# Optimization experiments

Measured on AMD Instinct MI355X. Metric: run time of the kernel, lower is better.

Reference implementation:

```python
import jax, jax.numpy as jnp
import numpy as np

EMBED_DIM = 1024
NUM_HEADS = 16
HEAD_DIM = EMBED_DIM // NUM_HEADS


def setup_inputs() -> dict:
    key = jax.random.key(0)
    ks = jax.random.split(key, 7)
    B, S, E = 2, 2048, EMBED_DIM
    # xavier_uniform bound for square [E, E] weight
    bound = float(np.sqrt(6.0 / (E + E)))
    mkw = lambda k: jax.random.uniform(k, (E, E), jnp.float32, -bound, bound)
    return {
        "query": jax.random.normal(ks[0], (B, S, E), jnp.float32),
        "key": jax.random.normal(ks[1], (B, S, E), jnp.float32),
        "value": jax.random.normal(ks[2], (B, S, E), jnp.float32),
        "Wq": mkw(ks[3]),
        "Wk": mkw(ks[4]),
        "Wv": mkw(ks[5]),
        "Wo": mkw(ks[6]),
    }


def reference(query, key, value, Wq, Wk, Wv, Wo):
    # Chunked sigmoid attention: since sigmoid has no cross-key normalization
    # and all projections are bias-free linear maps, summing per-KV-chunk
    # partial outputs is mathematically identical to the full computation:
    #   out = (sigmoid(scale * Q K^T) @ V) @ Wo^T
    B, L, E = query.shape
    H, D = NUM_HEADS, HEAD_DIM
    scale = D ** -0.5
    q = (query @ Wq.T).reshape(B, L, H, D) * scale   # [B,L,H,D]
    k = (key @ Wk.T).reshape(B, -1, H, D)            # [B,S,H,D]
    v = (value @ Wv.T).reshape(B, -1, H, D)          # [B,S,H,D]
    scores = jax.nn.sigmoid(jnp.einsum('blhd,bshd->bhls', q, k))  # [B,H,L,S]
    o = jnp.einsum('bhls,bshd->blhd', scores, v).reshape(B, L, E)
    return o @ Wo.T
```

## Files before the change

kernel.cpp:

```cpp
#include <hip/hip_runtime.h>

typedef float f32x4 __attribute__((ext_vector_type(4)));
typedef float f32x16 __attribute__((ext_vector_type(16)));
typedef __bf16 bf16x4 __attribute__((ext_vector_type(4)));
typedef __bf16 bf16x8 __attribute__((ext_vector_type(8)));

constexpr int E = 1024;
constexpr int S = 2048;
constexpr int Bsz = 2;
constexpr int H = 16;
constexpr int Dh = 64;
constexpr int M = Bsz * S;

#define GLOAD_LDS16(g, l)                                                                 \
  __builtin_amdgcn_global_load_lds((const __attribute__((address_space(1))) void*)(g),    \
                                   (__attribute__((address_space(3))) void*)(l), 16, 0, 0)

__device__ __forceinline__ unsigned pk2(float a, float b) {
  union { __bf16 h[2]; unsigned u; } r;
  r.h[0] = (__bf16)a; r.h[1] = (__bf16)b;
  return r.u;
}

__global__ __launch_bounds__(256) void convert_bf16(
    const float* __restrict__ q, const float* __restrict__ k,
    const float* __restrict__ v, const float* __restrict__ wq,
    const float* __restrict__ wk, const float* __restrict__ wv,
    const float* __restrict__ wo, __bf16* __restrict__ aq,
    __bf16* __restrict__ ak, __bf16* __restrict__ av,
    __bf16* __restrict__ wqkv, __bf16* __restrict__ wob) {
  const int id = blockIdx.y;
  const float* src;
  __bf16* dst;
  int n;
  float scale = 1.0f;
  switch (id) {
    case 0: src = q;  dst = aq;             n = M * E; break;
    case 1: src = k;  dst = ak;             n = M * E; break;
    case 2: src = v;  dst = av;             n = M * E; break;
    case 3: src = wq; dst = wqkv;           n = E * E; scale = -0.18033688f; break;
    case 4: src = wk; dst = wqkv + E * E;   n = E * E; break;
    case 5: src = wv; dst = wqkv + 2 * E * E; n = E * E; break;
    default: src = wo; dst = wob;           n = E * E; break;
  }
  const int stride = gridDim.x * 256 * 8;
  for (int i = (blockIdx.x * 256 + threadIdx.x) * 8; i < n; i += stride) {
    f32x4 a = *reinterpret_cast<const f32x4*>(&src[i]);
    f32x4 b = *reinterpret_cast<const f32x4*>(&src[i + 4]);
    bf16x8 o;
    o[0] = (__bf16)(a[0] * scale); o[1] = (__bf16)(a[1] * scale);
    o[2] = (__bf16)(a[2] * scale); o[3] = (__bf16)(a[3] * scale);
    o[4] = (__bf16)(b[0] * scale); o[5] = (__bf16)(b[1] * scale);
    o[6] = (__bf16)(b[2] * scale); o[7] = (__bf16)(b[3] * scale);
    *reinterpret_cast<bf16x8*>(&dst[i]) = o;
  }
}

template <int TM, int MODE>
__global__ __launch_bounds__(256) void gemm_bf16nt(
    const __bf16* __restrict__ A0, const __bf16* __restrict__ A1,
    const __bf16* __restrict__ A2, const __bf16* __restrict__ Bw,
    void* __restrict__ C0, void* __restrict__ C1, void* __restrict__ C2) {
  constexpr int MI = TM / 32;
  __shared__ __bf16 As[TM][64];
  __shared__ __bf16 Bs[128][64];

  const int t    = threadIdx.x;
  const int lane = t & 63;
  const int wid  = t >> 6;
  const int wr   = (wid >> 1) * (TM / 2);
  const int wc   = (wid & 1) * 64;
  const int r16  = lane & 15;
  const int tm   = blockIdx.y * TM;
  const int tn   = blockIdx.x * 128;
  const int which = tn >> 10;

  const __bf16* Ab = (MODE == 0) ? (which == 0 ? A0 : which == 1 ? A1 : A2) : A0;

  f32x4 acc[MI][4] = {};

  for (int kt = 0; kt < E / 64; ++kt) {
    const int k0 = kt * 64;
    __syncthreads();
    constexpr int ACH = TM / 8;
    constexpr int NCH = ACH + 16;
#pragma unroll
    for (int c = wid; c < NCH; c += 4) {
      const bool isA = c < ACH;
      const int cc   = isA ? c : c - ACH;
      const int L    = cc * 1024 + lane * 16;
      const int row  = L >> 7;
      const int sw   = ((L >> 4) & 7) ^ (row & 7);
      const __bf16* src = isA ? &Ab[(size_t)(tm + row) * E + k0 + sw * 8]
                              : &Bw[(size_t)(tn + row) * E + k0 + sw * 8];
      char* dst = (isA ? (char*)As : (char*)Bs) + cc * 1024;
      GLOAD_LDS16(src, dst);
    }
    __syncthreads();
#pragma unroll
    for (int kc = 0; kc < 2; ++kc) {
      bf16x8 af[MI], bfv[4];
#pragma unroll
      for (int mi = 0; mi < MI; ++mi) {
        int row = wr + mi * 16 + r16;
        int g   = (kc * 4 + (lane >> 4)) ^ (row & 7);
        af[mi] = *reinterpret_cast<const bf16x8*>(&As[row][g * 8]);
      }
#pragma unroll
      for (int ni = 0; ni < 4; ++ni) {
        int row = wc + ni * 16 + r16;
        int g   = (kc * 4 + (lane >> 4)) ^ (row & 7);
        bfv[ni] = *reinterpret_cast<const bf16x8*>(&Bs[row][g * 8]);
      }
#pragma unroll
      for (int mi = 0; mi < MI; ++mi)
#pragma unroll
        for (int ni = 0; ni < 4; ++ni)
          acc[mi][ni] = __builtin_amdgcn_mfma_f32_16x16x32_bf16(af[mi], bfv[ni],
                                                                acc[mi][ni], 0, 0, 0);
    }
  }

#pragma unroll
  for (int mi = 0; mi < MI; ++mi) {
#pragma unroll
    for (int ni = 0; ni < 4; ++ni) {
#pragma unroll
      for (int j = 0; j < 4; ++j) {
        float v = acc[mi][ni][j];
        int m = tm + wr + mi * 16 + ((lane >> 4) << 2) + j;
        int n = tn + wc + ni * 16 + r16;
        if constexpr (MODE == 0) {
          int nl = n & 1023;
          int b = m >> 11, s = m & 2047, h = nl >> 6, d = nl & 63;
          __bf16* Cout = which == 0 ? (__bf16*)C0 : which == 1 ? (__bf16*)C1
                                                              : (__bf16*)C2;
          if (which < 2) {
            Cout[((size_t)(b * H + h) * S + s) * Dh + d] = (__bf16)v;
          } else {
            int ssw = (s & ~12) | ((s & 4) << 1) | ((s & 8) >> 1);
            Cout[((size_t)(b * H + h) * Dh + d) * S + ssw] = (__bf16)v;
          }
        } else {
          ((float*)C0)[(size_t)m * E + n] = v;
        }
      }
    }
  }
}

__global__ __launch_bounds__(128) void attn_sigmoid(const __bf16* __restrict__ Q,
                                                    const __bf16* __restrict__ K,
                                                    const __bf16* __restrict__ Vt,
                                                    __bf16* __restrict__ O) {
  __shared__ char smem[2][16384];

  const int t    = threadIdx.x;
  const int lane = t & 63;
  const int wid  = t >> 6;
  const int l31  = lane & 31;
  const int hh   = lane >> 5;
  const int q0   = blockIdx.x * 64;
  const int h    = blockIdx.y;
  const int b    = blockIdx.z;

  const __bf16* Qh = Q + (size_t)(b * H + h) * S * Dh;
  const __bf16* Kh = K + (size_t)(b * H + h) * S * Dh;
  const __bf16* Vh = Vt + (size_t)(b * H + h) * Dh * S;

  auto stage = [&](int st, int pb) {
    char* bK = &smem[pb][0];
    char* bV = &smem[pb][8192];
#pragma unroll
    for (int j = 0; j < 4; ++j) {
      int base = (wid * 4 + j) * 1024;
      int L    = base + lane * 16;
      int row  = L >> 7;
      int sw   = ((L >> 4) & 7) ^ (row & 7);
      GLOAD_LDS16(&Kh[(size_t)(st * 64 + row) * Dh + sw * 8], bK + base);
      GLOAD_LDS16(&Vh[(size_t)row * S + st * 64 + sw * 8], bV + base);
    }
  };

  stage(0, 0);

  bf16x8 Qf[4];
#pragma unroll
  for (int kc = 0; kc < 4; ++kc)
    Qf[kc] = *reinterpret_cast<const bf16x8*>(
        &Qh[(size_t)(q0 + wid * 32 + l31) * Dh + kc * 16 + hh * 8]);

  f32x16 ot0 = {}, ot1 = {};
  __syncthreads();

  for (int st = 0; st < S / 64; ++st) {
    const int cur = st & 1;
    if (st + 1 < S / 64) stage(st + 1, cur ^ 1);

    const __bf16* Ks = (const __bf16*)&smem[cur][0];
    const __bf16* Vs = (const __bf16*)(&smem[cur][8192]);

    f32x16 s0 = {}, s1 = {};
    __builtin_amdgcn_s_setprio(1);
#pragma unroll
    for (int kc = 0; kc < 4; ++kc) {
      int x = (2 * kc + hh) ^ (l31 & 7);
      bf16x8 k0 = *reinterpret_cast<const bf16x8*>(&Ks[l31 * 64 + x * 8]);
      bf16x8 k1 = *reinterpret_cast<const bf16x8*>(&Ks[(32 + l31) * 64 + x * 8]);
      s0 = __builtin_amdgcn_mfma_f32_32x32x16_bf16(k0, Qf[kc], s0, 0, 0, 0);
      s1 = __builtin_amdgcn_mfma_f32_32x32x16_bf16(k1, Qf[kc], s1, 0, 0, 0);
    }
    __builtin_amdgcn_s_setprio(0);

    bf16x8 vf[8];
#pragma unroll
    for (int c = 0; c < 4; ++c) {
#pragma unroll
      for (int dblk = 0; dblk < 2; ++dblk) {
        int row = dblk * 32 + l31;
        int x   = (2 * c + hh) ^ (row & 7);
        vf[c * 2 + dblk] = *reinterpret_cast<const bf16x8*>(&Vs[row * 64 + x * 8]);
      }
    }

    bf16x8 F[4];
    {
      union { unsigned u[4]; bf16x8 v; } fu[4];
#pragma unroll
      for (int c = 0; c < 4; ++c) {
        int base = (c & 1) * 8;
#pragma unroll
        for (int jj = 0; jj < 4; ++jj) {
          float ya = (c < 2) ? s0[base + 2 * jj] : s1[base + 2 * jj];
          float yb = (c < 2) ? s0[base + 2 * jj + 1] : s1[base + 2 * jj + 1];
          float pa = __builtin_amdgcn_rcpf(1.0f + __builtin_amdgcn_exp2f(ya));
          float pb = __builtin_amdgcn_rcpf(1.0f + __builtin_amdgcn_exp2f(yb));
          fu[c].u[jj] = pk2(pa, pb);
        }
        F[c] = fu[c].v;
      }
    }

    __builtin_amdgcn_s_setprio(1);
#pragma unroll
    for (int c = 0; c < 4; ++c) {
      ot0 = __builtin_amdgcn_mfma_f32_32x32x16_bf16(vf[c * 2 + 0], F[c], ot0, 0, 0, 0);
      ot1 = __builtin_amdgcn_mfma_f32_32x32x16_bf16(vf[c * 2 + 1], F[c], ot1, 0, 0, 0);
    }
    __builtin_amdgcn_s_setprio(0);

    __syncthreads();
  }

  __bf16* Os = (__bf16*)&smem[0][0];
  {
    int row = wid * 32 + l31;
#pragma unroll
    for (int dblk = 0; dblk < 2; ++dblk) {
#pragma unroll
      for (int rp = 0; rp < 4; ++rp) {
        int r  = rp * 4;
        int g  = dblk * 4 + rp;
        int by = row * 128 + ((g ^ (row & 7)) * 16) + hh * 8;
        float a0 = dblk ? ot1[r]     : ot0[r];
        float a1 = dblk ? ot1[r + 1] : ot0[r + 1];
        float a2 = dblk ? ot1[r + 2] : ot0[r + 2];
        float a3 = dblk ? ot1[r + 3] : ot0[r + 3];
        unsigned long long val =
            (unsigned long long)pk2(a0, a1) | ((unsigned long long)pk2(a2, a3) << 32);
        *reinterpret_cast<unsigned long long*>((char*)Os + by) = val;
      }
    }
  }
  __syncthreads();
#pragma unroll
  for (int i = 0; i < 4; ++i) {
    int c   = i * 128 + t;
    int row = c >> 3;
    int ch  = c & 7;
    bf16x8 v = *reinterpret_cast<const bf16x8*>(
        (char*)Os + row * 128 + ((ch ^ (row & 7)) * 16));
    *reinterpret_cast<bf16x8*>(&O[((size_t)(b * S) + q0 + row) * E + h * Dh + ch * 8]) = v;
  }
}

extern "C" void kernel_launch(void* const* d_in, const int* in_sizes, int n_in,
                              void* d_out, int out_size, void* d_ws, size_t ws_size,
                              hipStream_t stream) {
  const float* query = (const float*)d_in[0];
  const float* key_  = (const float*)d_in[1];
  const float* value = (const float*)d_in[2];
  const float* Wq    = (const float*)d_in[3];
  const float* Wk    = (const float*)d_in[4];
  const float* Wv    = (const float*)d_in[5];
  const float* Wo    = (const float*)d_in[6];

  char* ws = (char*)d_ws;
  __bf16* aq   = (__bf16*)(ws);
  __bf16* ak   = (__bf16*)(ws + ((size_t)8 << 20));
  __bf16* av   = (__bf16*)(ws + ((size_t)16 << 20));
  __bf16* wqkv = (__bf16*)(ws + ((size_t)24 << 20));
  __bf16* wob  = (__bf16*)(ws + ((size_t)30 << 20));
  __bf16* pq   = (__bf16*)(ws + ((size_t)32 << 20));
  __bf16* pk   = (__bf16*)(ws + ((size_t)40 << 20));
  __bf16* pvt  = (__bf16*)(ws + ((size_t)48 << 20));
  __bf16* ob   = (__bf16*)(ws);

  convert_bf16<<<dim3(512, 7), 256, 0, stream>>>(query, key_, value, Wq, Wk, Wv,
                                                 Wo, aq, ak, av, wqkv, wob);

  gemm_bf16nt<128, 0><<<dim3(3072 / 128, M / 128), 256, 0, stream>>>(
      aq, ak, av, wqkv, pq, pk, pvt);

  attn_sigmoid<<<dim3(S / 64, H, Bsz), 128, 0, stream>>>(pq, pk, pvt, ob);

  gemm_bf16nt<64, 2><<<dim3(E / 128, M / 64), 256, 0, stream>>>(
      ob, nullptr, nullptr, wob, (float*)d_out, nullptr, nullptr);
}
```

Before: 154.3 us.

## Split attention key range across two wave pairs and reduce partial outputs in LDS

The attention block grows from 2 to 4 waves. Each pair of waves handles half of the key sequence in 32-key steps, and within a pair one wave loads K while the other loads V. At the end the partial outputs are summed through shared memory. This is meant to raise the number of resident waves and hide latency within each block, at the cost of a cross-wave reduction and smaller MFMA batches per iteration.

```diff
diff --git a/kernel.cpp b/kernel.cpp
--- a/kernel.cpp
+++ b/kernel.cpp
@@ -149,36 +149,44 @@
   }
 }
 
-__global__ __launch_bounds__(128) void attn_sigmoid(const __bf16* __restrict__ Q,
+__global__ __launch_bounds__(256) void attn_sigmoid(const __bf16* __restrict__ Q,
                                                     const __bf16* __restrict__ K,
                                                     const __bf16* __restrict__ Vt,
                                                     __bf16* __restrict__ O) {
-  __shared__ char smem[2][16384];
-
-  const int t    = threadIdx.x;
-  const int lane = t & 63;
-  const int wid  = t >> 6;
-  const int l31  = lane & 31;
-  const int hh   = lane >> 5;
-  const int q0   = blockIdx.x * 64;
-  const int h    = blockIdx.y;
-  const int b    = blockIdx.z;
+  __shared__ char smem[32768];
+
+  const int t     = threadIdx.x;
+  const int lane  = t & 63;
+  const int wid   = t >> 6;
+  const int l31   = lane & 31;
+  const int hh    = lane >> 5;
+  const int qgrp  = wid & 1;
+  const int shalf = wid >> 1;
+  const int q0    = blockIdx.x * 64;
+  const int h     = blockIdx.y;
+  const int b     = blockIdx.z;
 
   const __bf16* Qh = Q + (size_t)(b * H + h) * S * Dh;
   const __bf16* Kh = K + (size_t)(b * H + h) * S * Dh;
   const __bf16* Vh = Vt + (size_t)(b * H + h) * Dh * S;
 
-  auto stage = [&](int st, int pb) {
-    char* bK = &smem[pb][0];
-    char* bV = &smem[pb][8192];
-#pragma unroll
-    for (int j = 0; j < 4; ++j) {
-      int base = (wid * 4 + j) * 1024;
-      int L    = base + lane * 16;
-      int row  = L >> 7;
-      int sw   = ((L >> 4) & 7) ^ (row & 7);
-      GLOAD_LDS16(&Kh[(size_t)(st * 64 + row) * Dh + sw * 8], bK + base);
-      GLOAD_LDS16(&Vh[(size_t)row * S + st * 64 + sw * 8], bV + base);
+  char* const myBase = smem + shalf * 16384;
+
+  const __bf16* kSrc = Kh + (size_t)(shalf * 1024 + (lane >> 3)) * Dh +
+                       (((lane & 7) ^ (lane >> 3)) * 8);
+  const __bf16* vSrc = Vh + (size_t)(lane >> 2) * S + shalf * 1024 +
+                       (((lane & 3) ^ ((lane >> 3) & 3)) * 8);
+
+  auto stage = [&](int it, int buf) {
+    char* dst = myBase + buf * 8192;
+    if (qgrp == 0) {
+#pragma unroll
+      for (int j = 0; j < 4; ++j)
+        GLOAD_LDS16(kSrc + it * 2048 + j * 512, dst + j * 1024);
+    } else {
+#pragma unroll
+      for (int j = 0; j < 4; ++j)
+        GLOAD_LDS16(vSrc + it * 32 + (size_t)j * 16 * S, dst + 4096 + j * 1024);
     }
   };
 
@@ -188,75 +196,110 @@
 #pragma unroll
   for (int kc = 0; kc < 4; ++kc)
     Qf[kc] = *reinterpret_cast<const bf16x8*>(
-        &Qh[(size_t)(q0 + wid * 32 + l31) * Dh + kc * 16 + hh * 8]);
+        &Qh[(size_t)(q0 + qgrp * 32 + l31) * Dh + kc * 16 + hh * 8]);
 
   f32x16 ot0 = {}, ot1 = {};
   __syncthreads();
 
-  for (int st = 0; st < S / 64; ++st) {
-    const int cur = st & 1;
-    if (st + 1 < S / 64) stage(st + 1, cur ^ 1);
-
-    const __bf16* Ks = (const __bf16*)&smem[cur][0];
-    const __bf16* Vs = (const __bf16*)(&smem[cur][8192]);
-
-    f32x16 s0 = {}, s1 = {};
-    __builtin_amdgcn_s_setprio(1);
+#pragma unroll 2
+  for (int it = 0; it < 32; ++it) {
+    const int buf = it & 1;
+    if (it + 1 < 32) stage(it + 1, buf ^ 1);
+
+    const __bf16* Kb = (const __bf16*)(myBase + buf * 8192);
+    const __bf16* Vb = (const __bf16*)(myBase + buf * 8192 + 4096);
+
+    bf16x8 kf[4], vf[4];
 #pragma unroll
     for (int kc = 0; kc < 4; ++kc) {
       int x = (2 * kc + hh) ^ (l31 & 7);
-      bf16x8 k0 = *reinterpret_cast<const bf16x8*>(&Ks[l31 * 64 + x * 8]);
-      bf16x8 k1 = *reinterpret_cast<const bf16x8*>(&Ks[(32 + l31) * 64 + x * 8]);
-      s0 = __builtin_amdgcn_mfma_f32_32x32x16_bf16(k0, Qf[kc], s0, 0, 0, 0);
-      s1 = __builtin_amdgcn_mfma_f32_32x32x16_bf16(k1, Qf[kc], s1, 0, 0, 0);
-    }
-    __builtin_amdgcn_s_setprio(0);
-
-    bf16x8 vf[8];
-#pragma unroll
-    for (int c = 0; c < 4; ++c) {
+      kf[kc] = *reinterpret_cast<const bf16x8*>(&Kb[l31 * 64 + x * 8]);
+    }
+#pragma unroll
+    for (int kc2 = 0; kc2 < 2; ++kc2)
 #pragma unroll
       for (int dblk = 0; dblk < 2; ++dblk) {
         int row = dblk * 32 + l31;
-        int x   = (2 * c + hh) ^ (row & 7);
-        vf[c * 2 + dblk] = *reinterpret_cast<const bf16x8*>(&Vs[row * 64 + x * 8]);
-      }
-    }
-
-    bf16x8 F[4];
+        int x   = (2 * kc2 + hh) ^ ((l31 >> 1) & 3);
+        vf[kc2 * 2 + dblk] = *reinterpret_cast<const bf16x8*>(&Vb[row * 32 + x * 8]);
+      }
+
+    f32x16 sacc = {};
+    __builtin_amdgcn_s_setprio(1);
+#pragma unroll
+    for (int kc = 0; kc < 4; ++kc)
+      sacc = __builtin_amdgcn_mfma_f32_32x32x16_bf16(kf[kc], Qf[kc], sacc, 0, 0, 0);
+    __builtin_amdgcn_s_setprio(0);
+
+    bf16x8 F[2];
     {
-      union { unsigned u[4]; bf16x8 v; } fu[4];
-#pragma unroll
-      for (int c = 0; c < 4; ++c) {
-        int base = (c & 1) * 8;
+      union { unsigned u[4]; bf16x8 v; } fu[2];
+#pragma unroll
+      for (int kc2 = 0; kc2 < 2; ++kc2) {
 #pragma unroll
         for (int jj = 0; jj < 4; ++jj) {
-          float ya = (c < 2) ? s0[base + 2 * jj] : s1[base + 2 * jj];
-          float yb = (c < 2) ? s0[base + 2 * jj + 1] : s1[base + 2 * jj + 1];
+          float ya = sacc[kc2 * 8 + 2 * jj];
+          float yb = sacc[kc2 * 8 + 2 * jj + 1];
           float pa = __builtin_amdgcn_rcpf(1.0f + __builtin_amdgcn_exp2f(ya));
           float pb = __builtin_amdgcn_rcpf(1.0f + __builtin_amdgcn_exp2f(yb));
-          fu[c].u[jj] = pk2(pa, pb);
+          fu[kc2].u[jj] = pk2(pa, pb);
         }
-        F[c] = fu[c].v;
+        F[kc2] = fu[kc2].v;
       }
     }
 
     __builtin_amdgcn_s_setprio(1);
-#pragma unroll
-    for (int c = 0; c < 4; ++c) {
-      ot0 = __builtin_amdgcn_mfma_f32_32x32x16_bf16(vf[c * 2 + 0], F[c], ot0, 0, 0, 0);
-      ot1 = __builtin_amdgcn_mfma_f32_32x32x16_bf16(vf[c * 2 + 1], F[c], ot1, 0, 0, 0);
-    }
+    ot0 = __builtin_amdgcn_mfma_f32_32x32x16_bf16(vf[0], F[0], ot0, 0, 0, 0);
+    ot1 = __builtin_amdgcn_mfma_f32_32x32x16_bf16(vf[1], F[0], ot1, 0, 0, 0);
+    ot0 = __builtin_amdgcn_mfma_f32_32x32x16_bf16(vf[2], F[1], ot0, 0, 0, 0);
+    ot1 = __builtin_amdgcn_mfma_f32_32x32x16_bf16(vf[3], F[1], ot1, 0, 0, 0);
     __builtin_amdgcn_s_setprio(0);
 
     __syncthreads();
   }
 
-  __bf16* Os = (__bf16*)&smem[0][0];
+  const int q = qgrp * 32 + l31;
   {
-    int row = wid * 32 + l31;
-#pragma unroll
-    for (int dblk = 0; dblk < 2; ++dblk) {
+    char* Ps = smem;
+    if (shalf == 1) {
+#pragma unroll
+      for (int dblk = 0; dblk < 2; ++dblk)
+#pragma unroll
+        for (int rp = 0; rp < 4; ++rp) {
+          int gg = dblk * 8 + rp * 2 + hh;
+          int r  = rp * 4;
+          f32x4 v;
+          v[0] = dblk ? ot1[r]     : ot0[r];
+          v[1] = dblk ? ot1[r + 1] : ot0[r + 1];
+          v[2] = dblk ? ot1[r + 2] : ot0[r + 2];
+          v[3] = dblk ? ot1[r + 3] : ot0[r + 3];
+          *reinterpret_cast<f32x4*>(Ps + q * 256 + ((gg ^ (q & 7)) * 16)) = v;
+        }
+    }
+    __syncthreads();
+    if (shalf == 0) {
+#pragma unroll
+      for (int dblk = 0; dblk < 2; ++dblk)
+#pragma unroll
+        for (int rp = 0; rp < 4; ++rp) {
+          int gg = dblk * 8 + rp * 2 + hh;
+          int r  = rp * 4;
+          f32x4 v = *reinterpret_cast<const f32x4*>(Ps + q * 256 + ((gg ^ (q & 7)) * 16));
+          if (dblk) {
+            ot1[r] += v[0]; ot1[r + 1] += v[1]; ot1[r + 2] += v[2]; ot1[r + 3] += v[3];
+          } else {
+            ot0[r] += v[0]; ot0[r + 1] += v[1]; ot0[r + 2] += v[2]; ot0[r + 3] += v[3];
+          }
+        }
+    }
+  }
+  __syncthreads();
+
+  __bf16* Os = (__bf16*)smem;
+  if (shalf == 0) {
+    int row = q;
+#pragma unroll
+    for (int dblk = 0; dblk < 2; ++dblk)
 #pragma unroll
       for (int rp = 0; rp < 4; ++rp) {
         int r  = rp * 4;
@@ -270,12 +313,11 @@
             (unsigned long long)pk2(a0, a1) | ((unsigned long long)pk2(a2, a3) << 32);
         *reinterpret_cast<unsigned long long*>((char*)Os + by) = val;
       }
-    }
   }
   __syncthreads();
 #pragma unroll
-  for (int i = 0; i < 4; ++i) {
-    int c   = i * 128 + t;
+  for (int i = 0; i < 2; ++i) {
+    int c   = i * 256 + t;
     int row = c >> 3;
     int ch  = c & 7;
     bf16x8 v = *reinterpret_cast<const bf16x8*>(
@@ -312,7 +354,7 @@
   gemm_bf16nt<128, 0><<<dim3(3072 / 128, M / 128), 256, 0, stream>>>(
       aq, ak, av, wqkv, pq, pk, pvt);
 
-  attn_sigmoid<<<dim3(S / 64, H, Bsz), 128, 0, stream>>>(pq, pk, pvt, ob);
+  attn_sigmoid<<<dim3(S / 64, H, Bsz), 256, 0, stream>>>(pq, pk, pvt, ob);
 
   gemm_bf16nt<64, 2><<<dim3(E / 128, M / 64), 256, 0, stream>>>(
       ob, nullptr, nullptr, wob, (float*)d_out, nullptr, nullptr);
```

Measured after the change: 152.8 us. Within noise of the previous version (-1.0%).
